# Kernel optimization log

Hardware: AMD Instinct MI355X
Metric: run time of the kernel (lower is better)

Reference implementation:

```python
import jax, jax.numpy as jnp
import numpy as np

EPS = float(np.finfo(np.float32).eps)
NUM_PROP = 5          # config.model.num_prop
NUM_STEP_S2V = 3      # config.model.num_step_set2vec


def _gru_cell(x, h, wih, whh, bih, bhh):
    # PyTorch GRUCell: gate order r, z, n
    gi = x @ wih.T + bih
    gh = h @ whh.T + bhh
    ir, iz, in_ = jnp.split(gi, 3, axis=-1)
    hr, hz, hn = jnp.split(gh, 3, axis=-1)
    r = jax.nn.sigmoid(ir + hr)
    z = jax.nn.sigmoid(iz + hz)
    n = jnp.tanh(in_ + r * hn)
    return (1.0 - z) * n + z * h


def _lstm_cell(x, h, c, wih, whh, bih, bhh):
    # PyTorch LSTMCell: gate order i, f, g, o
    g = x @ wih.T + bih + h @ whh.T + bhh
    i, f, gg, o = jnp.split(g, 4, axis=-1)
    c2 = jax.nn.sigmoid(f) * c + jax.nn.sigmoid(i) * jnp.tanh(gg)
    return jax.nn.sigmoid(o) * jnp.tanh(c2), c2


def _set2vec(m, wih, whh, bih, bhh):
    # Set2Vec / set2set encoder (Vinyals et al. 2015) over a node set m: [N, H].
    # Returns q_star: [2H] = concat(LSTM hidden, attention read).
    H = m.shape[-1]
    h = jnp.zeros((H,), m.dtype)
    c = jnp.zeros((H,), m.dtype)
    q = jnp.zeros((2 * H,), m.dtype)
    for _ in range(NUM_STEP_S2V):
        h, c = _lstm_cell(q, h, c, wih, whh, bih, bhh)
        att = jax.nn.softmax(m @ h)   # [N] attention over set elements
        r = att @ m                   # [H] read vector
        q = jnp.concatenate([h, r])
    return q


def setup_inputs() -> dict:
    key = jax.random.key(0)
    ks = jax.random.split(key, 12)
    B, N, Da, Din, H, E1, Dout = 32, 512, 100, 64, 128, 4, 16
    s = 0.05
    return {
        "node_feat": jax.random.randint(ks[0], (B, N), 0, Da),
        "L": jax.random.randint(ks[1], (B, N, N, E1), 0, 2).astype(jnp.float32),
        "node_emb": jax.random.normal(ks[2], (Da, Din)) * s,
        "W_in": jax.random.normal(ks[3], (H, Din)) * s,
        "b_in": jnp.zeros((H,)),
        "edge_emb": jax.random.normal(ks[4], (E1, H * H)) * s,
        "gru_wih": jax.random.normal(ks[5], (3 * H, E1 * H)) * s,
        "gru_whh": jax.random.normal(ks[6], (3 * H, H)) * s,
        "gru_bih": jnp.zeros((3 * H,)),
        "gru_bhh": jnp.zeros((3 * H,)),
        "lstm_wih": jax.random.normal(ks[7], (4 * H, 2 * H)) * s,
        "lstm_whh": jax.random.normal(ks[8], (4 * H, H)) * s,
        "lstm_bih": jnp.zeros((4 * H,)),
        "lstm_bhh": jnp.zeros((4 * H,)),
        "W_out": jax.random.normal(ks[9], (Dout, 2 * H)) * s,
        "b_out": jnp.zeros((Dout,)),
    }


def reference(node_feat, L, node_emb, W_in, b_in, edge_emb,
              gru_wih, gru_whh, gru_bih, gru_bhh,
              lstm_wih, lstm_whh, lstm_bih, lstm_bhh,
              W_out, b_out):
    B, N = node_feat.shape
    H = W_in.shape[0]
    E1 = edge_emb.shape[0]
    # L[L != 0] = 1.0  (binarize adjacency)
    A = jnp.where(L != 0, 1.0, 0.0).astype(L.dtype)            # [B,N,N,E1]
    # node embedding + input linear
    state = node_emb[node_feat] @ W_in.T + b_in                # [B,N,H]
    Eop = edge_emb.reshape(E1, H, H)                           # per-edge-type operator
    for _ in range(NUM_PROP):
        # per-edge-type message: state @ edge_em  (all types at once)
        msg = jnp.einsum('bnh,ehk->bnek', state, Eop)          # [B,N,E1,H]
        # sum aggregation: bmm(A[...,e], msg_e)
        agg = jnp.einsum('bmne,bnek->bmek', A, msg)            # [B,N,E1,H]
        msg_cat = agg.reshape(B, N, E1 * H)                    # cat over edge types (dim=2)
        state = _gru_cell(msg_cat, state, gru_wih, gru_whh, gru_bih, gru_bhh)
        # dropout p=0.0 -> identity
    # Set2Vec per graph (mask=None path), then output linear
    q = jax.vmap(lambda s: _set2vec(s, lstm_wih, lstm_whh, lstm_bih, lstm_bhh))(state)  # [B,2H]
    return q @ W_out.T + b_out                                 # [B,Dout]
```

## Files before the change

### kernel.cpp

```cpp
#include <hip/hip_runtime.h>
#include <hip/hip_bf16.h>

#define BB 32
#define NN 512
#define DA 100
#define DIN 64
#define HH 128
#define E1 4
#define DOUT 16
#define NPROP 5
#define NS2V 3
#define MHALF 8192

typedef __attribute__((ext_vector_type(8))) short bf16x8;
typedef __attribute__((ext_vector_type(4))) float f32x4;
typedef __attribute__((ext_vector_type(4))) unsigned short us4;
typedef __attribute__((ext_vector_type(8))) unsigned short us8;
typedef unsigned short ushort_t;

__device__ __forceinline__ unsigned short f2bf(float f) {
    __hip_bfloat16 h = __float2bfloat16(f);
    return *reinterpret_cast<unsigned short*>(&h);
}
__device__ __forceinline__ float bf2f(unsigned short u) {
    unsigned v = ((unsigned)u) << 16;
    float f;
    __builtin_memcpy(&f, &v, 4);
    return f;
}

__global__ void pack_A_kernel(const float* __restrict__ L, unsigned* __restrict__ Abits) {
    int t = blockIdx.x * blockDim.x + threadIdx.x;
    if (t >= BB * NN * (NN / 32)) return;
    int w = t & 15;
    int m = (t >> 4) & (NN - 1);
    int b = t >> (4 + 9);
    const float* src = L + ((size_t)(b * NN + m) * NN + 32 * w) * E1;
    unsigned bits[E1] = {0u, 0u, 0u, 0u};
    #pragma unroll 8
    for (int j = 0; j < 32; ++j) {
        float4 v = *reinterpret_cast<const float4*>(src + j * 4);
        if (v.x != 0.f) bits[0] |= (1u << j);
        if (v.y != 0.f) bits[1] |= (1u << j);
        if (v.z != 0.f) bits[2] |= (1u << j);
        if (v.w != 0.f) bits[3] |= (1u << j);
    }
    #pragma unroll
    for (int e = 0; e < E1; ++e)
        Abits[((b * E1 + e) * NN + m) * 16 + w] = bits[e];
}

__global__ void convW_kernel(const float* __restrict__ EE, const float* __restrict__ wih,
                             const float* __restrict__ whh,
                             ushort_t* __restrict__ U_h, ushort_t* __restrict__ U_l,
                             ushort_t* __restrict__ whh_h, ushort_t* __restrict__ whh_l) {
    int t = blockIdx.x * blockDim.x + threadIdx.x;
    if (t < 384 * 512) {
        int col = t & 511;
        int j = t >> 9;
        int e = col >> 7, h = col & 127;
        const float4* wp = reinterpret_cast<const float4*>(wih + (size_t)j * 512 + e * 128);
        const float4* ep = reinterpret_cast<const float4*>(EE + (size_t)e * 16384 + h * 128);
        float acc = 0.f;
        #pragma unroll 8
        for (int k4 = 0; k4 < 32; ++k4) {
            float4 a = wp[k4], b = ep[k4];
            acc = fmaf(a.x, b.x, fmaf(a.y, b.y, fmaf(a.z, b.z, fmaf(a.w, b.w, acc))));
        }
        unsigned short hi = f2bf(acc);
        U_h[t] = hi;
        U_l[t] = f2bf(acc - bf2f(hi));
        return;
    }
    int t2 = t - 384 * 512;
    if (t2 < 384 * 128) {
        float v = whh[t2];
        unsigned short hi = f2bf(v);
        whh_h[t2] = hi;
        whh_l[t2] = f2bf(v - bf2f(hi));
    }
}

__global__ void embed_kernel(const int* __restrict__ nf, const float* __restrict__ emb,
                             const float* __restrict__ Win, const float* __restrict__ bin,
                             ushort_t* __restrict__ s_hi, ushort_t* __restrict__ s_lo) {
    int row = blockIdx.x;
    int h = threadIdx.x;
    __shared__ float e[DIN];
    int a = nf[row];
    if (h < DIN) e[h] = emb[a * DIN + h];
    __syncthreads();
    float acc = bin[h];
    const float* w = Win + h * DIN;
    #pragma unroll
    for (int d = 0; d < DIN; ++d) acc = fmaf(e[d], w[d], acc);
    unsigned short hi = f2bf(acc);
    s_hi[row * HH + h] = hi;
    s_lo[row * HH + h] = f2bf(acc - bf2f(hi));
}

__global__ __launch_bounds__(256) void transpose_kernel(const ushort_t* __restrict__ src,
                                                        ushort_t* __restrict__ dst,
                                                        size_t splane) {
    __shared__ __align__(16) ushort_t tile[128][72];
    int row0 = blockIdx.x * 64;
    int tid = threadIdx.x;
    #pragma unroll
    for (int pl = 0; pl < 2; ++pl) {
        const ushort_t* s = src + pl * splane;
        ushort_t* d = dst + pl * splane;
        #pragma unroll
        for (int q = 0; q < 4; ++q) {
            int idx = q * 256 + tid;
            int r = idx >> 4, h8 = idx & 15;
            bf16x8 v = *reinterpret_cast<const bf16x8*>(s + (size_t)(row0 + r) * HH + h8 * 8);
            #pragma unroll
            for (int j = 0; j < 8; ++j) tile[h8 * 8 + j][r] = (ushort_t)v[j];
        }
        __syncthreads();
        {
            int h = tid >> 1, rseg = (tid & 1) * 32;
            #pragma unroll
            for (int s8 = 0; s8 < 4; ++s8) {
                us8 v = *reinterpret_cast<const us8*>(&tile[h][rseg + s8 * 8]);
                *reinterpret_cast<us8*>(&d[(size_t)h * 16384 + row0 + rseg + s8 * 8]) = v;
            }
        }
        __syncthreads();
    }
}

template <int MODE, bool AGG, bool XBITS, int K, bool XSPLIT, bool WSPLIT>
__global__ __launch_bounds__(256) void mm_kernel(const void* __restrict__ Xp, size_t xplane,
                                                 const ushort_t* __restrict__ W, size_t wplane,
                                                 const float* __restrict__ bias,
                                                 void* __restrict__ outv, size_t oplane,
                                                 int ldx, int ldw, int ldo) {
    __shared__ __align__(16) ushort_t Xs[2][128 * 40];
    __shared__ __align__(16) ushort_t Ws[2][64 * 40];
    int tid = threadIdx.x;
    int row0 = blockIdx.y * 128, col0 = blockIdx.x * 64;
    const ushort_t* X = (const ushort_t*)Xp;
    const unsigned* Xb = (const unsigned*)Xp;
    size_t out_off = 0;
    int wko = 0;
    if constexpr (AGG) {
        int e = blockIdx.z & 3, bl = blockIdx.z >> 2;
        Xb += (size_t)blockIdx.z * NN * 16;
        wko = bl * NN;
        out_off = (size_t)bl * NN * NN + (size_t)e * HH;
    }
    int lane = tid & 63;
    int wave = tid >> 6;
    int wm = wave & 1, wn = wave >> 1;
    int r16 = lane & 15, kg = lane >> 4;

    f32x4 acc[4][2] = {};

    for (int k0 = 0; k0 < K; k0 += 32) {
        bf16x8 xh[2], xl[2];
        unsigned xword;
        if constexpr (XBITS) {
            int m = tid >> 1;
            xword = Xb[(size_t)(row0 + m) * 16 + (k0 >> 5)];
        } else {
            #pragma unroll
            for (int q = 0; q < 2; ++q) {
                int chunk = q * 256 + tid;
                int r = chunk >> 2, kc = chunk & 3;
                const ushort_t* xp = X + (size_t)(row0 + r) * ldx + k0 + kc * 8;
                xh[q] = *reinterpret_cast<const bf16x8*>(xp);
                if constexpr (XSPLIT) xl[q] = *reinterpret_cast<const bf16x8*>(xp + xplane);
            }
        }
        bf16x8 wh, wl;
        {
            int r = tid >> 2, kc = tid & 3;
            const ushort_t* wp2 = W + (size_t)(col0 + r) * ldw + wko + k0 + kc * 8;
            wh = *reinterpret_cast<const bf16x8*>(wp2);
            if constexpr (WSPLIT) wl = *reinterpret_cast<const bf16x8*>(wp2 + wplane);
        }
        __syncthreads();
        if constexpr (XBITS) {
            int m = tid >> 1, sel = tid & 1;
            #pragma unroll
            for (int j8 = 0; j8 < 2; ++j8) {
                bf16x8 xv;
                #pragma unroll
                for (int j = 0; j < 8; ++j)
                    xv[j] = (short)(((xword >> (sel * 16 + j8 * 8 + j)) & 1u) ? 0x3F80 : 0);
                *reinterpret_cast<bf16x8*>(&Xs[0][m * 40 + sel * 16 + j8 * 8]) = xv;
            }
        } else {
            #pragma unroll
            for (int q = 0; q < 2; ++q) {
                int chunk = q * 256 + tid;
                int r = chunk >> 2, kc = chunk & 3;
                *reinterpret_cast<bf16x8*>(&Xs[0][r * 40 + kc * 8]) = xh[q];
                if constexpr (XSPLIT)
                    *reinterpret_cast<bf16x8*>(&Xs[1][r * 40 + kc * 8]) = xl[q];
            }
        }
        {
            int r = tid >> 2, kc = tid & 3;
            *reinterpret_cast<bf16x8*>(&Ws[0][r * 40 + kc * 8]) = wh;
            if constexpr (WSPLIT)
                *reinterpret_cast<bf16x8*>(&Ws[1][r * 40 + kc * 8]) = wl;
        }
        __syncthreads();
        bf16x8 af_h[4], af_l[4], bf_h[2], bf_l[2];
        #pragma unroll
        for (int mi = 0; mi < 4; ++mi) {
            af_h[mi] = *reinterpret_cast<const bf16x8*>(&Xs[0][(wm * 64 + mi * 16 + r16) * 40 + kg * 8]);
            if constexpr (XSPLIT)
                af_l[mi] = *reinterpret_cast<const bf16x8*>(&Xs[1][(wm * 64 + mi * 16 + r16) * 40 + kg * 8]);
        }
        #pragma unroll
        for (int ni = 0; ni < 2; ++ni) {
            bf_h[ni] = *reinterpret_cast<const bf16x8*>(&Ws[0][(wn * 32 + ni * 16 + r16) * 40 + kg * 8]);
            if constexpr (WSPLIT)
                bf_l[ni] = *reinterpret_cast<const bf16x8*>(&Ws[1][(wn * 32 + ni * 16 + r16) * 40 + kg * 8]);
        }
        #pragma unroll
        for (int mi = 0; mi < 4; ++mi)
            #pragma unroll
            for (int ni = 0; ni < 2; ++ni) {
                acc[mi][ni] = __builtin_amdgcn_mfma_f32_16x16x32_bf16(af_h[mi], bf_h[ni], acc[mi][ni], 0, 0, 0);
                if constexpr (XSPLIT)
                    acc[mi][ni] = __builtin_amdgcn_mfma_f32_16x16x32_bf16(af_l[mi], bf_h[ni], acc[mi][ni], 0, 0, 0);
                if constexpr (WSPLIT)
                    acc[mi][ni] = __builtin_amdgcn_mfma_f32_16x16x32_bf16(af_h[mi], bf_l[ni], acc[mi][ni], 0, 0, 0);
            }
    }

    if constexpr (MODE == 3) {
        float* out = (float*)outv;
        #pragma unroll
        for (int ni = 0; ni < 2; ++ni) {
            int col = col0 + wn * 32 + ni * 16 + r16;
            float bv = bias[col];
            #pragma unroll
            for (int mi = 0; mi < 4; ++mi) {
                int rowb = row0 + wm * 64 + mi * 16 + kg * 4;
                #pragma unroll
                for (int j = 0; j < 4; ++j)
                    out[(size_t)(rowb + j) * ldo + col] = acc[mi][ni][j] + bv;
            }
        }
    } else {
        ushort_t* out = (ushort_t*)outv + out_off;
        #pragma unroll
        for (int ni = 0; ni < 2; ++ni) {
            int col = col0 + wn * 32 + ni * 16 + r16;
            #pragma unroll
            for (int mi = 0; mi < 4; ++mi) {
                int rowb = row0 + wm * 64 + mi * 16 + kg * 4;
                #pragma unroll
                for (int j = 0; j < 4; ++j) {
                    float v = acc[mi][ni][j];
                    unsigned short hv = f2bf(v);
                    out[(size_t)(rowb + j) * ldo + col] = hv;
                    out[oplane + (size_t)(rowb + j) * ldo + col] = f2bf(v - bf2f(hv));
                }
            }
        }
    }
}

__global__ void gru_gate_kernel(const float* __restrict__ gi, const float* __restrict__ gh,
                                ushort_t* __restrict__ s_hi, ushort_t* __restrict__ s_lo,
                                size_t half_off, int total) {
    int t = blockIdx.x * blockDim.x + threadIdx.x;
    if (t >= total) return;
    int row = t >> 7, j = t & 127;
    const float* gir = gi + (size_t)row * 384;
    const float* ghr = gh + (size_t)row * 384;
    float ir = gir[j], iz = gir[128 + j], in_ = gir[256 + j];
    float hr = ghr[j], hz = ghr[128 + j], hn = ghr[256 + j];
    float r = 1.f / (1.f + expf(-(ir + hr)));
    float z = 1.f / (1.f + expf(-(iz + hz)));
    float n = tanhf(in_ + r * hn);
    size_t g = half_off + (size_t)t;
    float h = bf2f(s_hi[g]) + bf2f(s_lo[g]);
    float v = (1.f - z) * n + z * h;
    unsigned short hv = f2bf(v);
    s_hi[g] = hv;
    s_lo[g] = f2bf(v - bf2f(hv));
}


__global__ __launch_bounds__(256) void s2v_g_kernel(int step,
        const float* __restrict__ hvec, const float* __restrict__ rpart,
        const float* __restrict__ wih, const float* __restrict__ whh,
        const float* __restrict__ bih, const float* __restrict__ bhh,
        float* __restrict__ g_all) {
    int b = blockIdx.y, tid = threadIdx.x;
    int j = blockIdx.x * 256 + tid;
    __shared__ float q[256];
    if (step > 0) {
        if (tid < 128) q[tid] = hvec[b * 128 + tid];
        else {
            int h2 = tid - 128;
            const float* rp = rpart + (size_t)b * 512;
            q[tid] = rp[h2] + rp[128 + h2] + rp[256 + h2] + rp[384 + h2];
        }
    } else {
        q[tid] = 0.f;
    }
    __syncthreads();
    float acc = bih[j] + bhh[j];
    if (step > 0) {
        const float4* wi = reinterpret_cast<const float4*>(wih + (size_t)j * 256);
        #pragma unroll 8
        for (int d4 = 0; d4 < 64; ++d4) {
            float4 w = wi[d4];
            acc = fmaf(q[d4 * 4 + 0], w.x, fmaf(q[d4 * 4 + 1], w.y,
                  fmaf(q[d4 * 4 + 2], w.z, fmaf(q[d4 * 4 + 3], w.w, acc))));
        }
        const float4* wp = reinterpret_cast<const float4*>(whh + (size_t)j * 128);
        #pragma unroll 8
        for (int d4 = 0; d4 < 32; ++d4) {
            float4 w = wp[d4];
            acc = fmaf(q[d4 * 4 + 0], w.x, fmaf(q[d4 * 4 + 1], w.y,
                  fmaf(q[d4 * 4 + 2], w.z, fmaf(q[d4 * 4 + 3], w.w, acc))));
        }
    }
    g_all[(size_t)b * 512 + j] = acc;
}

__global__ __launch_bounds__(256) void s2v_cl_kernel(int step,
        const float* __restrict__ g_all, float* __restrict__ cvec, float* __restrict__ hvec,
        const ushort_t* __restrict__ s_hi, const ushort_t* __restrict__ s_lo,
        float* __restrict__ logits) {
    int b = blockIdx.y, chunk = blockIdx.x, tid = threadIdx.x;
    __shared__ float hs[HH];
    if (tid < HH) {
        const float* g = g_all + (size_t)b * 512;
        float i_ = 1.f / (1.f + expf(-g[tid]));
        float f_ = 1.f / (1.f + expf(-g[128 + tid]));
        float g_ = tanhf(g[256 + tid]);
        float o_ = 1.f / (1.f + expf(-g[384 + tid]));
        float c0 = (step == 0) ? 0.f : cvec[b * 128 + tid];
        float c2 = f_ * c0 + i_ * g_;
        float hn = o_ * tanhf(c2);
        hs[tid] = hn;
        if (chunk == 0) { cvec[b * 128 + tid] = c2; hvec[b * 128 + tid] = hn; }
    }
    __syncthreads();
    int n = chunk * 256 + tid;
    const ushort_t* ph = s_hi + ((size_t)b * NN + n) * HH;
    const ushort_t* pl = s_lo + ((size_t)b * NN + n) * HH;
    float lg = 0.f;
    #pragma unroll
    for (int i8 = 0; i8 < 16; ++i8) {
        bf16x8 vh = *reinterpret_cast<const bf16x8*>(ph + i8 * 8);
        bf16x8 vl = *reinterpret_cast<const bf16x8*>(pl + i8 * 8);
        #pragma unroll
        for (int k = 0; k < 8; ++k)
            lg = fmaf(bf2f((ushort_t)vh[k]) + bf2f((ushort_t)vl[k]), hs[i8 * 8 + k], lg);
    }
    logits[(size_t)b * 512 + n] = lg;
}

__global__ __launch_bounds__(256) void s2v_read_kernel(const float* __restrict__ logits,
        const ushort_t* __restrict__ t_hi, const ushort_t* __restrict__ t_lo,
        float* __restrict__ rpart) {
    int b = blockIdx.y, chunk = blockIdx.x, tid = threadIdx.x;
    __shared__ float lgs[NN];
    __shared__ float att[128];
    __shared__ float wred[8];
    __shared__ float red[256];
    lgs[tid] = logits[(size_t)b * 512 + tid];
    lgs[256 + tid] = logits[(size_t)b * 512 + 256 + tid];
    __syncthreads();
    float mv = fmaxf(lgs[tid], lgs[tid + 256]);
    #pragma unroll
    for (int m = 32; m >= 1; m >>= 1) mv = fmaxf(mv, __shfl_xor(mv, m));
    if ((tid & 63) == 0) wred[tid >> 6] = mv;
    __syncthreads();
    float mx = fmaxf(fmaxf(wred[0], wred[1]), fmaxf(wred[2], wred[3]));
    float sv = expf(lgs[tid] - mx) + expf(lgs[tid + 256] - mx);
    #pragma unroll
    for (int m = 32; m >= 1; m >>= 1) sv += __shfl_xor(sv, m);
    if ((tid & 63) == 0) wred[4 + (tid >> 6)] = sv;
    __syncthreads();
    float inv = 1.f / (wred[4] + wred[5] + wred[6] + wred[7]);
    if (tid < 128) att[tid] = expf(lgs[chunk * 128 + tid] - mx) * inv;
    __syncthreads();
    int hh = tid & 127, half = tid >> 7;
    int colb = b * NN + chunk * 128 + half * 64;
    const ushort_t* ph = t_hi + (size_t)hh * 16384 + colb;
    const ushort_t* pl = t_lo + (size_t)hh * 16384 + colb;
    float racc = 0.f;
    #pragma unroll
    for (int i8 = 0; i8 < 8; ++i8) {
        bf16x8 vh = *reinterpret_cast<const bf16x8*>(ph + i8 * 8);
        bf16x8 vl = *reinterpret_cast<const bf16x8*>(pl + i8 * 8);
        #pragma unroll
        for (int k = 0; k < 8; ++k)
            racc = fmaf(att[half * 64 + i8 * 8 + k],
                        bf2f((ushort_t)vh[k]) + bf2f((ushort_t)vl[k]), racc);
    }
    red[tid] = racc;
    __syncthreads();
    if (tid < 128)
        rpart[(size_t)b * 512 + chunk * 128 + tid] = red[tid] + red[128 + tid];
}

__global__ __launch_bounds__(256) void s2v_out_kernel(const float* __restrict__ hvec,
        const float* __restrict__ rpart, const float* __restrict__ Wout,
        const float* __restrict__ bout, float* __restrict__ out) {
    int b = blockIdx.x, tid = threadIdx.x;
    __shared__ float q[256];
    if (tid < 128) q[tid] = hvec[b * 128 + tid];
    else {
        int h2 = tid - 128;
        const float* rp = rpart + (size_t)b * 512;
        q[tid] = rp[h2] + rp[128 + h2] + rp[256 + h2] + rp[384 + h2];
    }
    __syncthreads();
    if (tid < DOUT) {
        float acc = bout[tid];
        const float4* w = reinterpret_cast<const float4*>(Wout + (size_t)tid * 256);
        #pragma unroll 8
        for (int d4 = 0; d4 < 64; ++d4) {
            float4 wv = w[d4];
            acc = fmaf(q[d4 * 4 + 0], wv.x, fmaf(q[d4 * 4 + 1], wv.y,
                  fmaf(q[d4 * 4 + 2], wv.z, fmaf(q[d4 * 4 + 3], wv.w, acc))));
        }
        out[b * DOUT + tid] = acc;
    }
}

extern "C" void kernel_launch(void* const* d_in, const int* in_sizes, int n_in,
                              void* d_out, int out_size, void* d_ws, size_t ws_size,
                              hipStream_t stream) {
    const int*   node_feat = (const int*)d_in[0];
    const float* L         = (const float*)d_in[1];
    const float* node_emb  = (const float*)d_in[2];
    const float* W_in      = (const float*)d_in[3];
    const float* b_in      = (const float*)d_in[4];
    const float* edge_emb  = (const float*)d_in[5];
    const float* gru_wih   = (const float*)d_in[6];
    const float* gru_whh   = (const float*)d_in[7];
    const float* gru_bih   = (const float*)d_in[8];
    const float* gru_bhh   = (const float*)d_in[9];
    const float* lstm_wih  = (const float*)d_in[10];
    const float* lstm_whh  = (const float*)d_in[11];
    const float* lstm_bih  = (const float*)d_in[12];
    const float* lstm_bhh  = (const float*)d_in[13];
    const float* W_out     = (const float*)d_in[14];
    const float* b_out     = (const float*)d_in[15];
    float* out = (float*)d_out;

    char* ws = (char*)d_ws;
    const bool full = ws_size >= ((size_t)110 << 20);

    ushort_t* state_hi  = (ushort_t*)ws;
    ushort_t* stateT_hi = (ushort_t*)(ws + (8u << 20));
    unsigned* Abits     = (unsigned*)(ws + (16u << 20));
    ushort_t* S2        = (ushort_t*)(ws + (20u << 20));
    size_t s2plane      = full ? 8388608u : 4194304u;
    float*    gi        = (float*)(ws + (full ? (52ull << 20) : (36ull << 20)));
    float*    gh        = (float*)(ws + (full ? (76ull << 20) : (48ull << 20)));
    ushort_t* U_h       = (ushort_t*)(ws + (full ? (100ull << 20) : (60ull << 20)));
    ushort_t* U_l       = U_h + 196608;
    ushort_t* whh_h     = U_l + 196608;
    ushort_t* whh_l     = whh_h + 49152;
    float*    s2v       = (float*)(ws + (full ? (101ull << 20) : (61ull << 20)));
    float*    g_all     = s2v;
    float*    logits    = s2v + 16384;
    float*    hvec      = s2v + 32768;
    float*    cvec      = s2v + 36864;
    float*    rpart     = s2v + 40960;

    const size_t SPLANE = 2097152;

    pack_A_kernel<<<(BB * NN * 16) / 256, 256, 0, stream>>>(L, Abits);
    convW_kernel<<<(384 * 512 + 384 * 128) / 256, 256, 0, stream>>>(
        edge_emb, gru_wih, gru_whh, U_h, U_l, whh_h, whh_l);
    embed_kernel<<<BB * NN, 128, 0, stream>>>(node_feat, node_emb, W_in, b_in,
                                              state_hi, state_hi + SPLANE);

    const int nh   = full ? 1 : 2;
    const int zdim = full ? 128 : 64;
    const int ydim = full ? 128 : 64;
    const int rows = full ? 16384 : MHALF;

    for (int p = 0; p < NPROP; ++p) {
        transpose_kernel<<<256, 256, 0, stream>>>(state_hi, stateT_hi, SPLANE);
        for (int half = 0; half < nh; ++half) {
            const unsigned* Ab = Abits + (size_t)half * 16 * E1 * NN * 16;
            mm_kernel<4, true, true, 512, false, true><<<dim3(2, 4, zdim), 256, 0, stream>>>(
                Ab, 0, stateT_hi + (size_t)half * MHALF, SPLANE, nullptr,
                S2, s2plane, 0, 16384, 512);
            mm_kernel<3, false, false, 512, true, true><<<dim3(6, ydim), 256, 0, stream>>>(
                S2, s2plane, U_h, 196608, gru_bih, gi, 0, 512, 512, 384);
            mm_kernel<3, false, false, 128, true, true><<<dim3(6, ydim), 256, 0, stream>>>(
                state_hi + (size_t)half * MHALF * HH, SPLANE, whh_h, 49152, gru_bhh,
                gh, 0, 128, 128, 384);
            gru_gate_kernel<<<(rows * HH) / 256, 256, 0, stream>>>(
                gi, gh, state_hi, state_hi + SPLANE,
                (size_t)half * MHALF * HH, rows * HH);
        }
    }
    transpose_kernel<<<256, 256, 0, stream>>>(state_hi, stateT_hi, SPLANE);

    for (int step = 0; step < NS2V; ++step) {
        s2v_g_kernel<<<dim3(2, BB), 256, 0, stream>>>(step, hvec, rpart,
                                                      lstm_wih, lstm_whh, lstm_bih, lstm_bhh,
                                                      g_all);
        s2v_cl_kernel<<<dim3(2, BB), 256, 0, stream>>>(step, g_all, cvec, hvec,
                                                       state_hi, state_hi + SPLANE, logits);
        s2v_read_kernel<<<dim3(4, BB), 256, 0, stream>>>(logits, stateT_hi,
                                                         stateT_hi + SPLANE, rpart);
    }
    s2v_out_kernel<<<BB, 256, 0, stream>>>(hvec, rpart, W_out, b_out, out);
}
```

Before: 680.3 us.

## Fuse GRU input/hidden GEMMs into one launch and fold transpose into gate kernel

```diff
diff --git a/kernel.cpp b/kernel.cpp
--- a/kernel.cpp
+++ b/kernel.cpp
@@ -267,25 +267,158 @@
     }
 }
 
-__global__ void gru_gate_kernel(const float* __restrict__ gi, const float* __restrict__ gh,
-                                ushort_t* __restrict__ s_hi, ushort_t* __restrict__ s_lo,
-                                size_t half_off, int total) {
-    int t = blockIdx.x * blockDim.x + threadIdx.x;
-    if (t >= total) return;
-    int row = t >> 7, j = t & 127;
-    const float* gir = gi + (size_t)row * 384;
-    const float* ghr = gh + (size_t)row * 384;
-    float ir = gir[j], iz = gir[128 + j], in_ = gir[256 + j];
-    float hr = ghr[j], hz = ghr[128 + j], hn = ghr[256 + j];
-    float r = 1.f / (1.f + expf(-(ir + hr)));
-    float z = 1.f / (1.f + expf(-(iz + hz)));
-    float n = tanhf(in_ + r * hn);
-    size_t g = half_off + (size_t)t;
-    float h = bf2f(s_hi[g]) + bf2f(s_lo[g]);
-    float v = (1.f - z) * n + z * h;
-    unsigned short hv = f2bf(v);
-    s_hi[g] = hv;
-    s_lo[g] = f2bf(v - bf2f(hv));
+__global__ __launch_bounds__(256) void gigh_kernel(
+        const ushort_t* __restrict__ S2p, size_t s2pl,
+        const ushort_t* __restrict__ Sp, size_t spl,
+        const ushort_t* __restrict__ Up, size_t upl,
+        const ushort_t* __restrict__ Whp, size_t whpl,
+        const float* __restrict__ bih, const float* __restrict__ bhh,
+        float* __restrict__ gip, float* __restrict__ ghp) {
+    __shared__ __align__(16) ushort_t Xs[2][128 * 40];
+    __shared__ __align__(16) ushort_t Ws[2][64 * 40];
+    int tid = threadIdx.x;
+    int row0 = blockIdx.y * 128;
+    const ushort_t* X; const ushort_t* W; const float* bias; float* out;
+    size_t xplane, wplane; int ld, Kr, col0;
+    if (blockIdx.x < 6) {
+        X = S2p; xplane = s2pl; W = Up; wplane = upl; bias = bih; out = gip;
+        ld = 512; Kr = 512; col0 = blockIdx.x * 64;
+    } else {
+        X = Sp; xplane = spl; W = Whp; wplane = whpl; bias = bhh; out = ghp;
+        ld = 128; Kr = 128; col0 = (blockIdx.x - 6) * 64;
+    }
+    int lane = tid & 63, wave = tid >> 6;
+    int wm = wave & 1, wn = wave >> 1;
+    int r16 = lane & 15, kg = lane >> 4;
+
+    f32x4 acc[4][2] = {};
+
+    for (int k0 = 0; k0 < Kr; k0 += 32) {
+        bf16x8 xh[2], xl[2], wh, wl;
+        #pragma unroll
+        for (int q = 0; q < 2; ++q) {
+            int chunk = q * 256 + tid;
+            int r = chunk >> 2, kc = chunk & 3;
+            const ushort_t* xp = X + (size_t)(row0 + r) * ld + k0 + kc * 8;
+            xh[q] = *reinterpret_cast<const bf16x8*>(xp);
+            xl[q] = *reinterpret_cast<const bf16x8*>(xp + xplane);
+        }
+        {
+            int r = tid >> 2, kc = tid & 3;
+            const ushort_t* wp2 = W + (size_t)(col0 + r) * ld + k0 + kc * 8;
+            wh = *reinterpret_cast<const bf16x8*>(wp2);
+            wl = *reinterpret_cast<const bf16x8*>(wp2 + wplane);
+        }
+        __syncthreads();
+        #pragma unroll
+        for (int q = 0; q < 2; ++q) {
+            int chunk = q * 256 + tid;
+            int r = chunk >> 2, kc = chunk & 3;
+            *reinterpret_cast<bf16x8*>(&Xs[0][r * 40 + kc * 8]) = xh[q];
+            *reinterpret_cast<bf16x8*>(&Xs[1][r * 40 + kc * 8]) = xl[q];
+        }
+        {
+            int r = tid >> 2, kc = tid & 3;
+            *reinterpret_cast<bf16x8*>(&Ws[0][r * 40 + kc * 8]) = wh;
+            *reinterpret_cast<bf16x8*>(&Ws[1][r * 40 + kc * 8]) = wl;
+        }
+        __syncthreads();
+        bf16x8 af_h[4], af_l[4], bf_h[2], bf_l[2];
+        #pragma unroll
+        for (int mi = 0; mi < 4; ++mi) {
+            af_h[mi] = *reinterpret_cast<const bf16x8*>(&Xs[0][(wm * 64 + mi * 16 + r16) * 40 + kg * 8]);
+            af_l[mi] = *reinterpret_cast<const bf16x8*>(&Xs[1][(wm * 64 + mi * 16 + r16) * 40 + kg * 8]);
+        }
+        #pragma unroll
+        for (int ni = 0; ni < 2; ++ni) {
+            bf_h[ni] = *reinterpret_cast<const bf16x8*>(&Ws[0][(wn * 32 + ni * 16 + r16) * 40 + kg * 8]);
+            bf_l[ni] = *reinterpret_cast<const bf16x8*>(&Ws[1][(wn * 32 + ni * 16 + r16) * 40 + kg * 8]);
+        }
+        #pragma unroll
+        for (int mi = 0; mi < 4; ++mi)
+            #pragma unroll
+            for (int ni = 0; ni < 2; ++ni) {
+                acc[mi][ni] = __builtin_amdgcn_mfma_f32_16x16x32_bf16(af_h[mi], bf_h[ni], acc[mi][ni], 0, 0, 0);
+                acc[mi][ni] = __builtin_amdgcn_mfma_f32_16x16x32_bf16(af_l[mi], bf_h[ni], acc[mi][ni], 0, 0, 0);
+                acc[mi][ni] = __builtin_amdgcn_mfma_f32_16x16x32_bf16(af_h[mi], bf_l[ni], acc[mi][ni], 0, 0, 0);
+            }
+    }
+
+    #pragma unroll
+    for (int ni = 0; ni < 2; ++ni) {
+        int col = col0 + wn * 32 + ni * 16 + r16;
+        float bv = bias[col];
+        #pragma unroll
+        for (int mi = 0; mi < 4; ++mi) {
+            int rowb = row0 + wm * 64 + mi * 16 + kg * 4;
+            #pragma unroll
+            for (int j = 0; j < 4; ++j)
+                out[(size_t)(rowb + j) * 384 + col] = acc[mi][ni][j] + bv;
+        }
+    }
+}
+
+__global__ __launch_bounds__(256) void gate_t_kernel(const float* __restrict__ gi,
+        const float* __restrict__ gh,
+        ushort_t* __restrict__ s_hi, ushort_t* __restrict__ s_lo,
+        ushort_t* __restrict__ t_hi, ushort_t* __restrict__ t_lo, int row_base) {
+    __shared__ __align__(16) ushort_t th[HH][24];
+    __shared__ __align__(16) ushort_t tl[HH][24];
+    int tid = threadIdx.x;
+    int r_loc = tid >> 4;
+    int j0 = (tid & 15) * 8;
+    int row_l = blockIdx.x * 16 + r_loc;
+    size_t grow = (size_t)(row_base + row_l);
+    const float* gir = gi + (size_t)row_l * 384;
+    const float* ghr = gh + (size_t)row_l * 384;
+    ushort_t* sh = s_hi + grow * HH;
+    ushort_t* sl = s_lo + grow * HH;
+    __align__(16) ushort_t hb[8], lb[8];
+    #pragma unroll
+    for (int g4 = 0; g4 < 2; ++g4) {
+        int j = j0 + g4 * 4;
+        float4 ir4 = *reinterpret_cast<const float4*>(gir + j);
+        float4 iz4 = *reinterpret_cast<const float4*>(gir + 128 + j);
+        float4 in4 = *reinterpret_cast<const float4*>(gir + 256 + j);
+        float4 hr4 = *reinterpret_cast<const float4*>(ghr + j);
+        float4 hz4 = *reinterpret_cast<const float4*>(ghr + 128 + j);
+        float4 hn4 = *reinterpret_cast<const float4*>(ghr + 256 + j);
+        us4 oh4 = *reinterpret_cast<const us4*>(sh + j);
+        us4 ol4 = *reinterpret_cast<const us4*>(sl + j);
+        const float* irp = reinterpret_cast<const float*>(&ir4);
+        const float* izp = reinterpret_cast<const float*>(&iz4);
+        const float* inp = reinterpret_cast<const float*>(&in4);
+        const float* hrp = reinterpret_cast<const float*>(&hr4);
+        const float* hzp = reinterpret_cast<const float*>(&hz4);
+        const float* hnp = reinterpret_cast<const float*>(&hn4);
+        #pragma unroll
+        for (int c = 0; c < 4; ++c) {
+            float r = 1.f / (1.f + expf(-(irp[c] + hrp[c])));
+            float z = 1.f / (1.f + expf(-(izp[c] + hzp[c])));
+            float n = tanhf(inp[c] + r * hnp[c]);
+            float h = bf2f(oh4[c]) + bf2f(ol4[c]);
+            float v = (1.f - z) * n + z * h;
+            unsigned short hv = f2bf(v);
+            hb[g4 * 4 + c] = hv;
+            lb[g4 * 4 + c] = f2bf(v - bf2f(hv));
+        }
+    }
+    *reinterpret_cast<us8*>(sh + j0) = *reinterpret_cast<us8*>(&hb[0]);
+    *reinterpret_cast<us8*>(sl + j0) = *reinterpret_cast<us8*>(&lb[0]);
+    #pragma unroll
+    for (int k = 0; k < 8; ++k) {
+        th[j0 + k][r_loc] = hb[k];
+        tl[j0 + k][r_loc] = lb[k];
+    }
+    __syncthreads();
+    {
+        int j = tid >> 1, seg = (tid & 1) * 8;
+        size_t colb = (size_t)row_base + (size_t)blockIdx.x * 16 + seg;
+        *reinterpret_cast<us8*>(t_hi + (size_t)j * 16384 + colb) =
+            *reinterpret_cast<const us8*>(&th[j][seg]);
+        *reinterpret_cast<us8*>(t_lo + (size_t)j * 16384 + colb) =
+            *reinterpret_cast<const us8*>(&tl[j][seg]);
+    }
 }
 
 
@@ -481,6 +614,7 @@
         edge_emb, gru_wih, gru_whh, U_h, U_l, whh_h, whh_l);
     embed_kernel<<<BB * NN, 128, 0, stream>>>(node_feat, node_emb, W_in, b_in,
                                               state_hi, state_hi + SPLANE);
+    transpose_kernel<<<256, 256, 0, stream>>>(state_hi, stateT_hi, SPLANE);
 
     const int nh   = full ? 1 : 2;
     const int zdim = full ? 128 : 64;
@@ -488,23 +622,21 @@
     const int rows = full ? 16384 : MHALF;
 
     for (int p = 0; p < NPROP; ++p) {
-        transpose_kernel<<<256, 256, 0, stream>>>(state_hi, stateT_hi, SPLANE);
         for (int half = 0; half < nh; ++half) {
             const unsigned* Ab = Abits + (size_t)half * 16 * E1 * NN * 16;
             mm_kernel<4, true, true, 512, false, true><<<dim3(2, 4, zdim), 256, 0, stream>>>(
                 Ab, 0, stateT_hi + (size_t)half * MHALF, SPLANE, nullptr,
                 S2, s2plane, 0, 16384, 512);
-            mm_kernel<3, false, false, 512, true, true><<<dim3(6, ydim), 256, 0, stream>>>(
-                S2, s2plane, U_h, 196608, gru_bih, gi, 0, 512, 512, 384);
-            mm_kernel<3, false, false, 128, true, true><<<dim3(6, ydim), 256, 0, stream>>>(
-                state_hi + (size_t)half * MHALF * HH, SPLANE, whh_h, 49152, gru_bhh,
-                gh, 0, 128, 128, 384);
-            gru_gate_kernel<<<(rows * HH) / 256, 256, 0, stream>>>(
+            gigh_kernel<<<dim3(12, ydim), 256, 0, stream>>>(
+                S2, s2plane,
+                state_hi + (size_t)half * MHALF * HH, SPLANE,
+                U_h, 196608, whh_h, 49152,
+                gru_bih, gru_bhh, gi, gh);
+            gate_t_kernel<<<rows / 16, 256, 0, stream>>>(
                 gi, gh, state_hi, state_hi + SPLANE,
-                (size_t)half * MHALF * HH, rows * HH);
-        }
-    }
-    transpose_kernel<<<256, 256, 0, stream>>>(state_hi, stateT_hi, SPLANE);
+                stateT_hi, stateT_hi + SPLANE, half * MHALF);
+        }
+    }
 
     for (int step = 0; step < NS2V; ++step) {
         s2v_g_kernel<<<dim3(2, BB), 256, 0, stream>>>(step, hvec, rpart,
```

New measurement: 723.9 us. 6.4% more time.
